# Kernel optimization log

Hardware: AMD Instinct MI355X
Metric: run time of the kernel (lower is better)

## Reference

```python
import jax, jax.numpy as jnp
import numpy as np

N_LAT, N_LON = 721, 1440
N_MESH = 40962
C_IN, N_FEAT = 64, 4
HID, OUT = 256, 256
BATCH = 2


def _precompute_interp(mesh_lat, mesh_lon):
    """Vectorized version of BilinearInterpolator.__init__ precompute."""
    lat_min, lon_min = -np.pi / 2, 0.0
    dlat = np.pi / (N_LAT - 1)
    dlon = 2 * np.pi / N_LON
    lon = np.mod(mesh_lon - lon_min, 2 * np.pi) + lon_min
    lat_idx = (mesh_lat - lat_min) / dlat
    lon_idx = (lon - lon_min) / dlon
    i0 = np.clip(np.floor(lat_idx).astype(np.int64), 0, N_LAT - 2)
    j0 = np.clip(np.floor(lon_idx).astype(np.int64), 0, N_LON - 2)
    i1 = i0 + 1
    j1 = (j0 + 1) % N_LON
    lf = np.clip(lat_idx - i0, 0.0, 1.0)
    jf = np.clip(lon_idx - j0, 0.0, 1.0)
    idx = np.stack([i0 * N_LON + j0, i0 * N_LON + j1,
                    i1 * N_LON + j0, i1 * N_LON + j1], axis=1)
    w = np.stack([(1 - lf) * (1 - jf), (1 - lf) * jf,
                  lf * (1 - jf), lf * jf], axis=1).astype(np.float32)
    return idx, w


def setup_inputs() -> dict:
    key = jax.random.key(0)
    k = jax.random.split(key, 6)
    rng = np.random.default_rng(0)
    mesh_lat = rng.uniform(-np.pi / 2 + 1e-3, np.pi / 2 - 1e-3, N_MESH)
    mesh_lon = rng.uniform(0.0, 2 * np.pi, N_MESH)
    idx, w = _precompute_interp(mesh_lat, mesh_lon)
    d_in = C_IN + N_FEAT
    return {
        "grid_data": jax.random.normal(k[0], (BATCH, N_LAT, N_LON, C_IN), jnp.float32),
        "mesh_features": jax.random.normal(k[1], (N_MESH, N_FEAT), jnp.float32),
        "indices": jnp.asarray(idx, jnp.int64 if jax.config.read('jax_enable_x64') else jnp.int32),
        "weights": jnp.asarray(w),
        "W1": jax.random.normal(k[2], (d_in, HID), jnp.float32) / np.sqrt(d_in),
        "b1": jnp.zeros((HID,), jnp.float32),
        "W2": jax.random.normal(k[3], (HID, OUT), jnp.float32) / np.sqrt(HID),
        "b2": jnp.zeros((OUT,), jnp.float32),
    }


def reference(grid_data, mesh_features, indices, weights, W1, b1, W2, b2):
    B, n_lat, n_lon, C = grid_data.shape
    grid_flat = grid_data.reshape(B, n_lat * n_lon, C)          # (B, G, C)
    corner = grid_flat[:, indices, :]                           # (B, M, 4, C)
    mesh_data = jnp.einsum('bmkc,mk->bmc', corner, weights)     # weighted 4-pt sum
    mf = jnp.broadcast_to(mesh_features[None], (B,) + mesh_features.shape)
    combined = jnp.concatenate([mesh_data, mf], axis=-1)        # (B, M, C+F)
    h = jax.nn.relu(combined @ W1 + b1)                         # 2-layer MLP
    return h @ W2 + b2                                          # (B, M, OUT)
```

## Files before the change

kernel.cpp:

```cpp
#include <hip/hip_runtime.h>
#include <hip/hip_bf16.h>


constexpr int kNLat  = 721;
constexpr int kNLon  = 1440;
constexpr long long kNPix = (long long)kNLat * kNLon;
constexpr int kMesh  = 40962;
constexpr int kCIn   = 64;
constexpr int kFeat  = 4;
constexpr int kDIn   = kCIn + kFeat;
constexpr int kHid   = 256;
constexpr int kOut   = 256;
constexpr int kBatch = 2;

constexpr int kPts    = kBatch * kMesh;
constexpr int kPtsPad = (kPts + 63) & ~63;

typedef __attribute__((ext_vector_type(8))) short bf16x8;
typedef __attribute__((ext_vector_type(4))) float f32x4;

constexpr int    WSA1_N   = 16 * 3 * 64 * 8;
constexpr int    WSB2_N   = 16 * 8 * 64 * 8;
constexpr size_t WS_BYTES = (size_t)(WSA1_N + WSB2_N) * 2;

constexpr int MP    = 64;
constexpr int NBLKB = kPtsPad / MP;
constexpr int CSTR  = 104;
constexpr int HSTR  = 264;

__device__ inline ushort f2b(float v) {
    __hip_bfloat16 h = __float2bfloat16(v);
    return *reinterpret_cast<ushort*>(&h);
}

__global__ __launch_bounds__(256)
void g2m_prep(const float* __restrict__ W1, const float* __restrict__ W2,
              ushort* __restrict__ ws) {
    const int tid = blockIdx.x * 256 + threadIdx.x;
    if (tid < 3072) {
        const int l  = tid & 63;
        const int g  = tid >> 6;
        const int ks = g % 3;
        const int rt = g / 3;
        const int hid = rt * 16 + (l & 15);
        const int k0  = ks * 32 + (l >> 4) * 8;
        ushort tmp[8];
        #pragma unroll
        for (int j = 0; j < 8; ++j) {
            const int k = k0 + j;
            tmp[j] = f2b(k < kDIn ? W1[(size_t)k * kHid + hid] : 0.f);
        }
        *reinterpret_cast<bf16x8*>(ws + (size_t)tid * 8) =
            *reinterpret_cast<bf16x8*>(tmp);
    } else if (tid < 11264) {
        const int q  = tid - 3072;
        const int l  = q & 63;
        const int g  = q >> 6;
        const int ks = g % 8;
        const int ct = g / 8;
        const int col = ct * 16 + (l & 15);
        const int k0  = ks * 32 + (l >> 4) * 8;
        ushort tmp[8];
        #pragma unroll
        for (int j = 0; j < 8; ++j) {
            const int k = k0 + j;
            tmp[j] = f2b(W2[(size_t)k * kOut + col]);
        }
        *reinterpret_cast<bf16x8*>(ws + (size_t)(WSA1_N + q * 8)) =
            *reinterpret_cast<bf16x8*>(tmp);
    }
}

__global__ __launch_bounds__(256, 3)
void g2m_fused2(const float* __restrict__ grid,
                const float* __restrict__ mfeat,
                const int*   __restrict__ indices,
                const float* __restrict__ weights,
                const float* __restrict__ b1,
                const float* __restrict__ b2,
                const ushort* __restrict__ ws,
                float* __restrict__ out)
{
    __shared__ __align__(16) ushort comb[MP * CSTR];
    __shared__ __align__(16) ushort hbuf[MP * HSTR];

    const int t    = threadIdx.x;
    const int lane = t & 63;
    const int w    = t >> 6;
    const int p0   = blockIdx.x * MP;
    const int l15  = lane & 15;
    const int l4   = lane >> 4;

    {
        const int q = l4;
        #pragma unroll
        for (int it = 0; it < 4; ++it) {
            const int row = (w * 4 + it) * 4 + q;
            const int p   = p0 + row;
            float4 acc = {0.f, 0.f, 0.f, 0.f};
            float mf0 = 0.f, mf1 = 0.f;
            if (p < kPts) {
                const int b = (p >= kMesh) ? 1 : 0;
                const int m = p - b * kMesh;
                const int4   id = *reinterpret_cast<const int4*>(indices + (size_t)m * 4);
                const float4 wt = *reinterpret_cast<const float4*>(weights + (size_t)m * 4);
                const float* gb = grid + (size_t)b * (size_t)(kNPix * kCIn);
                const float4 r0 = *reinterpret_cast<const float4*>(gb + (size_t)id.x * kCIn + l15 * 4);
                const float4 r1 = *reinterpret_cast<const float4*>(gb + (size_t)id.y * kCIn + l15 * 4);
                const float4 r2 = *reinterpret_cast<const float4*>(gb + (size_t)id.z * kCIn + l15 * 4);
                const float4 r3 = *reinterpret_cast<const float4*>(gb + (size_t)id.w * kCIn + l15 * 4);
                acc.x = fmaf(wt.x, r0.x, fmaf(wt.y, r1.x, fmaf(wt.z, r2.x, wt.w * r3.x)));
                acc.y = fmaf(wt.x, r0.y, fmaf(wt.y, r1.y, fmaf(wt.z, r2.y, wt.w * r3.y)));
                acc.z = fmaf(wt.x, r0.z, fmaf(wt.y, r1.z, fmaf(wt.z, r2.z, wt.w * r3.z)));
                acc.w = fmaf(wt.x, r0.w, fmaf(wt.y, r1.w, fmaf(wt.z, r2.w, wt.w * r3.w)));
                if (l15 < 2) {
                    mf0 = mfeat[(size_t)m * kFeat + l15 * 2];
                    mf1 = mfeat[(size_t)m * kFeat + l15 * 2 + 1];
                }
            }
            ushort* rowp = &comb[row * CSTR];
            ushort4 pk;
            pk.x = f2b(acc.x); pk.y = f2b(acc.y); pk.z = f2b(acc.z); pk.w = f2b(acc.w);
            *reinterpret_cast<ushort4*>(rowp + l15 * 4) = pk;
            ushort2 ft;
            ft.x = f2b(mf0); ft.y = f2b(mf1);
            *reinterpret_cast<ushort2*>(rowp + 64 + l15 * 2) = ft;
        }
    }
    __syncthreads();

    {
        f32x4 acc1[4][4];
        #pragma unroll
        for (int r = 0; r < 4; ++r)
            #pragma unroll
            for (int mt = 0; mt < 4; ++mt) acc1[r][mt] = (f32x4)0.f;

        #pragma unroll
        for (int ks = 0; ks < 3; ++ks) {
            bf16x8 af[4], bfr[4];
            #pragma unroll
            for (int r = 0; r < 4; ++r) {
                const int rt = w * 4 + r;
                af[r] = *reinterpret_cast<const bf16x8*>(
                            ws + (size_t)((rt * 3 + ks) * 64 + lane) * 8);
            }
            #pragma unroll
            for (int mt = 0; mt < 4; ++mt)
                bfr[mt] = *reinterpret_cast<const bf16x8*>(
                            &comb[(mt * 16 + l15) * CSTR + ks * 32 + l4 * 8]);
            #pragma unroll
            for (int r = 0; r < 4; ++r)
                #pragma unroll
                for (int mt = 0; mt < 4; ++mt)
                    acc1[r][mt] = __builtin_amdgcn_mfma_f32_16x16x32_bf16(
                                      af[r], bfr[mt], acc1[r][mt], 0, 0, 0);
        }

        #pragma unroll
        for (int r = 0; r < 4; ++r) {
            const int hid0 = (w * 4 + r) * 16 + l4 * 4;
            const float4 bv = *reinterpret_cast<const float4*>(b1 + hid0);
            #pragma unroll
            for (int mt = 0; mt < 4; ++mt) {
                const int m = mt * 16 + l15;
                ushort4 hv;
                hv.x = f2b(fmaxf(acc1[r][mt][0] + bv.x, 0.f));
                hv.y = f2b(fmaxf(acc1[r][mt][1] + bv.y, 0.f));
                hv.z = f2b(fmaxf(acc1[r][mt][2] + bv.z, 0.f));
                hv.w = f2b(fmaxf(acc1[r][mt][3] + bv.w, 0.f));
                *reinterpret_cast<ushort4*>(&hbuf[m * HSTR + hid0]) = hv;
            }
        }
    }
    __syncthreads();

    {
        f32x4 acc2[4][4];
        #pragma unroll
        for (int mt = 0; mt < 4; ++mt)
            #pragma unroll
            for (int c = 0; c < 4; ++c) acc2[mt][c] = (f32x4)0.f;

        #pragma unroll
        for (int ks = 0; ks < 8; ++ks) {
            bf16x8 hf[4], wf[4];
            #pragma unroll
            for (int mt = 0; mt < 4; ++mt)
                hf[mt] = *reinterpret_cast<const bf16x8*>(
                            &hbuf[(mt * 16 + l15) * HSTR + ks * 32 + l4 * 8]);
            #pragma unroll
            for (int c = 0; c < 4; ++c) {
                const int ct = w * 4 + c;
                wf[c] = *reinterpret_cast<const bf16x8*>(
                            ws + (size_t)(WSA1_N + ((ct * 8 + ks) * 64 + lane) * 8));
            }
            #pragma unroll
            for (int mt = 0; mt < 4; ++mt)
                #pragma unroll
                for (int c = 0; c < 4; ++c)
                    acc2[mt][c] = __builtin_amdgcn_mfma_f32_16x16x32_bf16(
                                      wf[c], hf[mt], acc2[mt][c], 0, 0, 0);
        }

        #pragma unroll
        for (int c = 0; c < 4; ++c) {
            const int col0 = (w * 4 + c) * 16 + l4 * 4;
            const float4 bv = *reinterpret_cast<const float4*>(b2 + col0);
            #pragma unroll
            for (int mt = 0; mt < 4; ++mt) {
                const int p = p0 + mt * 16 + l15;
                if (p < kPts) {
                    float4 o;
                    o.x = acc2[mt][c][0] + bv.x;
                    o.y = acc2[mt][c][1] + bv.y;
                    o.z = acc2[mt][c][2] + bv.z;
                    o.w = acc2[mt][c][3] + bv.w;
                    *reinterpret_cast<float4*>(out + (size_t)p * kOut + col0) = o;
                }
            }
        }
    }
}

extern "C" void kernel_launch(void* const* d_in, const int* in_sizes, int n_in,
                              void* d_out, int out_size, void* d_ws, size_t ws_size,
                              hipStream_t stream) {
    const float* grid    = (const float*)d_in[0];
    const float* mfeat   = (const float*)d_in[1];
    const int*   indices = (const int*)d_in[2];
    const float* weights = (const float*)d_in[3];
    const float* W1      = (const float*)d_in[4];
    const float* b1      = (const float*)d_in[5];
    const float* W2      = (const float*)d_in[6];
    const float* b2      = (const float*)d_in[7];
    float* o = (float*)d_out;

    if (ws_size >= WS_BYTES) {
        ushort* ws = (ushort*)d_ws;
        g2m_prep<<<44, 256, 0, stream>>>(W1, W2, ws);
        g2m_fused2<<<NBLKB, 256, 0, stream>>>(grid, mfeat, indices, weights,
                                              b1, b2, ws, o);
    }
}
```

Measured before the change: 51.81 us.

## Gather interpolated inputs straight into MFMA B-fragments and swizzle hidden buffer

Each wave now gathers and interpolates its own 16 mesh points directly into the register layout of the layer-1 MFMA B operand. This removes the comb shared-memory staging buffer and one barrier. Each wave then computes all 16 hidden row-tiles for its points, which means every wave reads the full W1 fragment set rather than a quarter of it. The hidden buffer drops its padding in favour of an XOR swizzle to avoid LDS bank conflicts, and the launch bound is raised to 4 blocks per CU to fit the lower LDS and register use.

```diff
diff --git a/kernel.cpp b/kernel.cpp
--- a/kernel.cpp
+++ b/kernel.cpp
@@ -25,13 +25,14 @@
 
 constexpr int MP    = 64;
 constexpr int NBLKB = kPtsPad / MP;
-constexpr int CSTR  = 104;
-constexpr int HSTR  = 264;
+constexpr int HSTR  = 256;
 
 __device__ inline ushort f2b(float v) {
     __hip_bfloat16 h = __float2bfloat16(v);
     return *reinterpret_cast<ushort*>(&h);
 }
+
+__device__ inline int hswz(int r, int c) { return r * HSTR + (c ^ ((r & 7) << 3)); }
 
 __global__ __launch_bounds__(256)
 void g2m_prep(const float* __restrict__ W1, const float* __restrict__ W2,
@@ -71,8 +72,8 @@
     }
 }
 
-__global__ __launch_bounds__(256, 3)
-void g2m_fused2(const float* __restrict__ grid,
+__global__ __launch_bounds__(256, 4)
+void g2m_fused4(const float* __restrict__ grid,
                 const float* __restrict__ mfeat,
                 const int*   __restrict__ indices,
                 const float* __restrict__ weights,
@@ -81,7 +82,6 @@
                 const ushort* __restrict__ ws,
                 float* __restrict__ out)
 {
-    __shared__ __align__(16) ushort comb[MP * CSTR];
     __shared__ __align__(16) ushort hbuf[MP * HSTR];
 
     const int t    = threadIdx.x;
@@ -91,86 +91,81 @@
     const int l15  = lane & 15;
     const int l4   = lane >> 4;
 
+    bf16x8 bA[3];
     {
-        const int q = l4;
-        #pragma unroll
-        for (int it = 0; it < 4; ++it) {
-            const int row = (w * 4 + it) * 4 + q;
-            const int p   = p0 + row;
-            float4 acc = {0.f, 0.f, 0.f, 0.f};
-            float mf0 = 0.f, mf1 = 0.f;
-            if (p < kPts) {
-                const int b = (p >= kMesh) ? 1 : 0;
-                const int m = p - b * kMesh;
-                const int4   id = *reinterpret_cast<const int4*>(indices + (size_t)m * 4);
-                const float4 wt = *reinterpret_cast<const float4*>(weights + (size_t)m * 4);
-                const float* gb = grid + (size_t)b * (size_t)(kNPix * kCIn);
-                const float4 r0 = *reinterpret_cast<const float4*>(gb + (size_t)id.x * kCIn + l15 * 4);
-                const float4 r1 = *reinterpret_cast<const float4*>(gb + (size_t)id.y * kCIn + l15 * 4);
-                const float4 r2 = *reinterpret_cast<const float4*>(gb + (size_t)id.z * kCIn + l15 * 4);
-                const float4 r3 = *reinterpret_cast<const float4*>(gb + (size_t)id.w * kCIn + l15 * 4);
-                acc.x = fmaf(wt.x, r0.x, fmaf(wt.y, r1.x, fmaf(wt.z, r2.x, wt.w * r3.x)));
-                acc.y = fmaf(wt.x, r0.y, fmaf(wt.y, r1.y, fmaf(wt.z, r2.y, wt.w * r3.y)));
-                acc.z = fmaf(wt.x, r0.z, fmaf(wt.y, r1.z, fmaf(wt.z, r2.z, wt.w * r3.z)));
-                acc.w = fmaf(wt.x, r0.w, fmaf(wt.y, r1.w, fmaf(wt.z, r2.w, wt.w * r3.w)));
-                if (l15 < 2) {
-                    mf0 = mfeat[(size_t)m * kFeat + l15 * 2];
-                    mf1 = mfeat[(size_t)m * kFeat + l15 * 2 + 1];
-                }
+        const int p = p0 + w * 16 + l15;
+        float4 r0a{0,0,0,0}, r0b{0,0,0,0}, r0c{0,0,0,0}, r0d{0,0,0,0};
+        float4 r1a{0,0,0,0}, r1b{0,0,0,0}, r1c{0,0,0,0}, r1d{0,0,0,0};
+        float4 r2a{0,0,0,0}, r2b{0,0,0,0}, r2c{0,0,0,0}, r2d{0,0,0,0};
+        float4 r3a{0,0,0,0}, r3b{0,0,0,0}, r3c{0,0,0,0}, r3d{0,0,0,0};
+        float4 wt{0,0,0,0}, mfv{0,0,0,0};
+        if (p < kPts) {
+            const int b = (p >= kMesh) ? 1 : 0;
+            const int m = p - b * kMesh;
+            const int4 id = *reinterpret_cast<const int4*>(indices + (size_t)m * 4);
+            wt = *reinterpret_cast<const float4*>(weights + (size_t)m * 4);
+            const float* gb = grid + (size_t)b * (size_t)(kNPix * kCIn);
+            const int o0 = l4 * 8;
+            const int o1 = 32 + l4 * 8;
+            const float* c0 = gb + (size_t)id.x * kCIn;
+            const float* c1 = gb + (size_t)id.y * kCIn;
+            const float* c2 = gb + (size_t)id.z * kCIn;
+            const float* c3 = gb + (size_t)id.w * kCIn;
+            r0a = *reinterpret_cast<const float4*>(c0 + o0);
+            r0b = *reinterpret_cast<const float4*>(c0 + o0 + 4);
+            r0c = *reinterpret_cast<const float4*>(c0 + o1);
+            r0d = *reinterpret_cast<const float4*>(c0 + o1 + 4);
+            r1a = *reinterpret_cast<const float4*>(c1 + o0);
+            r1b = *reinterpret_cast<const float4*>(c1 + o0 + 4);
+            r1c = *reinterpret_cast<const float4*>(c1 + o1);
+            r1d = *reinterpret_cast<const float4*>(c1 + o1 + 4);
+            r2a = *reinterpret_cast<const float4*>(c2 + o0);
+            r2b = *reinterpret_cast<const float4*>(c2 + o0 + 4);
+            r2c = *reinterpret_cast<const float4*>(c2 + o1);
+            r2d = *reinterpret_cast<const float4*>(c2 + o1 + 4);
+            r3a = *reinterpret_cast<const float4*>(c3 + o0);
+            r3b = *reinterpret_cast<const float4*>(c3 + o0 + 4);
+            r3c = *reinterpret_cast<const float4*>(c3 + o1);
+            r3d = *reinterpret_cast<const float4*>(c3 + o1 + 4);
+            if (l4 == 0) mfv = *reinterpret_cast<const float4*>(mfeat + (size_t)m * 4);
+        }
+        ushort f0[8], f1[8], f2[8];
+        #pragma unroll
+        for (int j = 0; j < 4; ++j) {
+            const float a0 = (&r0a.x)[j], a1 = (&r1a.x)[j], a2 = (&r2a.x)[j], a3 = (&r3a.x)[j];
+            f0[j] = f2b(fmaf(wt.x, a0, fmaf(wt.y, a1, fmaf(wt.z, a2, wt.w * a3))));
+            const float b0 = (&r0b.x)[j], b1v = (&r1b.x)[j], b2v = (&r2b.x)[j], b3 = (&r3b.x)[j];
+            f0[4 + j] = f2b(fmaf(wt.x, b0, fmaf(wt.y, b1v, fmaf(wt.z, b2v, wt.w * b3))));
+            const float c0v = (&r0c.x)[j], c1v = (&r1c.x)[j], c2v = (&r2c.x)[j], c3v = (&r3c.x)[j];
+            f1[j] = f2b(fmaf(wt.x, c0v, fmaf(wt.y, c1v, fmaf(wt.z, c2v, wt.w * c3v))));
+            const float d0 = (&r0d.x)[j], d1 = (&r1d.x)[j], d2 = (&r2d.x)[j], d3 = (&r3d.x)[j];
+            f1[4 + j] = f2b(fmaf(wt.x, d0, fmaf(wt.y, d1, fmaf(wt.z, d2, wt.w * d3))));
+            f2[j]     = f2b((&mfv.x)[j]);
+            f2[4 + j] = 0;
+        }
+        bA[0] = *reinterpret_cast<bf16x8*>(f0);
+        bA[1] = *reinterpret_cast<bf16x8*>(f1);
+        bA[2] = *reinterpret_cast<bf16x8*>(f2);
+    }
+
+    {
+        #pragma unroll
+        for (int rt = 0; rt < 16; ++rt) {
+            f32x4 acc = (f32x4)0.f;
+            #pragma unroll
+            for (int ks = 0; ks < 3; ++ks) {
+                const bf16x8 af = *reinterpret_cast<const bf16x8*>(
+                        ws + (size_t)((rt * 3 + ks) * 64 + lane) * 8);
+                acc = __builtin_amdgcn_mfma_f32_16x16x32_bf16(af, bA[ks], acc, 0, 0, 0);
             }
-            ushort* rowp = &comb[row * CSTR];
-            ushort4 pk;
-            pk.x = f2b(acc.x); pk.y = f2b(acc.y); pk.z = f2b(acc.z); pk.w = f2b(acc.w);
-            *reinterpret_cast<ushort4*>(rowp + l15 * 4) = pk;
-            ushort2 ft;
-            ft.x = f2b(mf0); ft.y = f2b(mf1);
-            *reinterpret_cast<ushort2*>(rowp + 64 + l15 * 2) = ft;
-        }
-    }
-    __syncthreads();
-
-    {
-        f32x4 acc1[4][4];
-        #pragma unroll
-        for (int r = 0; r < 4; ++r)
-            #pragma unroll
-            for (int mt = 0; mt < 4; ++mt) acc1[r][mt] = (f32x4)0.f;
-
-        #pragma unroll
-        for (int ks = 0; ks < 3; ++ks) {
-            bf16x8 af[4], bfr[4];
-            #pragma unroll
-            for (int r = 0; r < 4; ++r) {
-                const int rt = w * 4 + r;
-                af[r] = *reinterpret_cast<const bf16x8*>(
-                            ws + (size_t)((rt * 3 + ks) * 64 + lane) * 8);
-            }
-            #pragma unroll
-            for (int mt = 0; mt < 4; ++mt)
-                bfr[mt] = *reinterpret_cast<const bf16x8*>(
-                            &comb[(mt * 16 + l15) * CSTR + ks * 32 + l4 * 8]);
-            #pragma unroll
-            for (int r = 0; r < 4; ++r)
-                #pragma unroll
-                for (int mt = 0; mt < 4; ++mt)
-                    acc1[r][mt] = __builtin_amdgcn_mfma_f32_16x16x32_bf16(
-                                      af[r], bfr[mt], acc1[r][mt], 0, 0, 0);
-        }
-
-        #pragma unroll
-        for (int r = 0; r < 4; ++r) {
-            const int hid0 = (w * 4 + r) * 16 + l4 * 4;
+            const int hid0 = rt * 16 + l4 * 4;
             const float4 bv = *reinterpret_cast<const float4*>(b1 + hid0);
-            #pragma unroll
-            for (int mt = 0; mt < 4; ++mt) {
-                const int m = mt * 16 + l15;
-                ushort4 hv;
-                hv.x = f2b(fmaxf(acc1[r][mt][0] + bv.x, 0.f));
-                hv.y = f2b(fmaxf(acc1[r][mt][1] + bv.y, 0.f));
-                hv.z = f2b(fmaxf(acc1[r][mt][2] + bv.z, 0.f));
-                hv.w = f2b(fmaxf(acc1[r][mt][3] + bv.w, 0.f));
-                *reinterpret_cast<ushort4*>(&hbuf[m * HSTR + hid0]) = hv;
-            }
+            ushort4 hv;
+            hv.x = f2b(fmaxf(acc[0] + bv.x, 0.f));
+            hv.y = f2b(fmaxf(acc[1] + bv.y, 0.f));
+            hv.z = f2b(fmaxf(acc[2] + bv.z, 0.f));
+            hv.w = f2b(fmaxf(acc[3] + bv.w, 0.f));
+            *reinterpret_cast<ushort4*>(&hbuf[hswz(w * 16 + l15, hid0)]) = hv;
         }
     }
     __syncthreads();
@@ -188,7 +183,7 @@
             #pragma unroll
             for (int mt = 0; mt < 4; ++mt)
                 hf[mt] = *reinterpret_cast<const bf16x8*>(
-                            &hbuf[(mt * 16 + l15) * HSTR + ks * 32 + l4 * 8]);
+                            &hbuf[hswz(mt * 16 + l15, ks * 32 + l4 * 8)]);
             #pragma unroll
             for (int c = 0; c < 4; ++c) {
                 const int ct = w * 4 + c;
@@ -239,7 +234,7 @@
     if (ws_size >= WS_BYTES) {
         ushort* ws = (ushort*)d_ws;
         g2m_prep<<<44, 256, 0, stream>>>(W1, W2, ws);
-        g2m_fused2<<<NBLKB, 256, 0, stream>>>(grid, mfeat, indices, weights,
+        g2m_fused4<<<NBLKB, 256, 0, stream>>>(grid, mfeat, indices, weights,
                                               b1, b2, ws, o);
     }
 }
```

Result: slower. 55.91 us (+7.9%).

## Warp-specialize into gather producers and MFMA consumers with double-buffered tiles

Applied to the files above, without the earlier changes.

Replaces the one-tile-per-block fused kernel with a persistent 512-thread kernel over 512 blocks. Four producer waves gather and interpolate the next 64-point tile into a second shared buffer while four consumer waves run both MLP GEMMs on the current tile. Each block handles 2 or 3 tiles. The aim is to hide the random-gather latency behind MFMA work. In exchange, half the waves issue the gathers, tile counts per block are uneven, and each tile step needs two block-wide barriers. The padding columns of the staging buffer are also zeroed explicitly.

```diff
diff --git a/kernel.cpp b/kernel.cpp
--- a/kernel.cpp
+++ b/kernel.cpp
@@ -23,10 +23,11 @@
 constexpr int    WSB2_N   = 16 * 8 * 64 * 8;
 constexpr size_t WS_BYTES = (size_t)(WSA1_N + WSB2_N) * 2;
 
-constexpr int MP    = 64;
-constexpr int NBLKB = kPtsPad / MP;
-constexpr int CSTR  = 104;
-constexpr int HSTR  = 264;
+constexpr int MP     = 64;
+constexpr int NTILES = kPtsPad / MP;
+constexpr int NBLK   = 512;
+constexpr int CSTR   = 104;
+constexpr int HSTR   = 264;
 
 __device__ inline ushort f2b(float v) {
     __hip_bfloat16 h = __float2bfloat16(v);
@@ -71,155 +72,220 @@
     }
 }
 
-__global__ __launch_bounds__(256, 3)
-void g2m_fused2(const float* __restrict__ grid,
-                const float* __restrict__ mfeat,
-                const int*   __restrict__ indices,
-                const float* __restrict__ weights,
-                const float* __restrict__ b1,
-                const float* __restrict__ b2,
-                const ushort* __restrict__ ws,
-                float* __restrict__ out)
+struct PState {
+    float4 rr[4][4];
+    float4 wt[4];
+    float  mf0[4], mf1[4];
+};
+
+__device__ inline void prod_load(const float* __restrict__ grid,
+                                 const float* __restrict__ mfeat,
+                                 const int*   __restrict__ indices,
+                                 const float* __restrict__ weights,
+                                 int p0, int pw, int l15, int l4, PState& s) {
+    #pragma unroll
+    for (int it = 0; it < 4; ++it) {
+        const int p = p0 + pw * 16 + it * 4 + l4;
+        s.rr[it][0] = s.rr[it][1] = s.rr[it][2] = s.rr[it][3] = float4{0.f, 0.f, 0.f, 0.f};
+        s.wt[it] = float4{0.f, 0.f, 0.f, 0.f};
+        s.mf0[it] = 0.f; s.mf1[it] = 0.f;
+        if (p < kPts) {
+            const int b = (p >= kMesh) ? 1 : 0;
+            const int m = p - b * kMesh;
+            const int4 id = *reinterpret_cast<const int4*>(indices + (size_t)m * 4);
+            s.wt[it] = *reinterpret_cast<const float4*>(weights + (size_t)m * 4);
+            const float* gb = grid + (size_t)b * (size_t)(kNPix * kCIn);
+            s.rr[it][0] = *reinterpret_cast<const float4*>(gb + (size_t)id.x * kCIn + l15 * 4);
+            s.rr[it][1] = *reinterpret_cast<const float4*>(gb + (size_t)id.y * kCIn + l15 * 4);
+            s.rr[it][2] = *reinterpret_cast<const float4*>(gb + (size_t)id.z * kCIn + l15 * 4);
+            s.rr[it][3] = *reinterpret_cast<const float4*>(gb + (size_t)id.w * kCIn + l15 * 4);
+            if (l15 < 2) {
+                s.mf0[it] = mfeat[(size_t)m * kFeat + l15 * 2];
+                s.mf1[it] = mfeat[(size_t)m * kFeat + l15 * 2 + 1];
+            }
+        }
+    }
+}
+
+__device__ inline void prod_reduce(const PState& s, ushort* comb,
+                                   int pw, int l15, int l4) {
+    #pragma unroll
+    for (int it = 0; it < 4; ++it) {
+        const int row = pw * 16 + it * 4 + l4;
+        const float4 wt = s.wt[it];
+        float4 acc;
+        acc.x = fmaf(wt.x, s.rr[it][0].x, fmaf(wt.y, s.rr[it][1].x, fmaf(wt.z, s.rr[it][2].x, wt.w * s.rr[it][3].x)));
+        acc.y = fmaf(wt.x, s.rr[it][0].y, fmaf(wt.y, s.rr[it][1].y, fmaf(wt.z, s.rr[it][2].y, wt.w * s.rr[it][3].y)));
+        acc.z = fmaf(wt.x, s.rr[it][0].z, fmaf(wt.y, s.rr[it][1].z, fmaf(wt.z, s.rr[it][2].z, wt.w * s.rr[it][3].z)));
+        acc.w = fmaf(wt.x, s.rr[it][0].w, fmaf(wt.y, s.rr[it][1].w, fmaf(wt.z, s.rr[it][2].w, wt.w * s.rr[it][3].w)));
+        ushort4 pk;
+        pk.x = f2b(acc.x); pk.y = f2b(acc.y); pk.z = f2b(acc.z); pk.w = f2b(acc.w);
+        *reinterpret_cast<ushort4*>(&comb[row * CSTR + l15 * 4]) = pk;
+        ushort2 ft;
+        ft.x = f2b(s.mf0[it]); ft.y = f2b(s.mf1[it]);
+        *reinterpret_cast<ushort2*>(&comb[row * CSTR + 64 + l15 * 2]) = ft;
+        if (l15 < (CSTR - kDIn) / 2 && l15 >= 0) {  }
+    }
+    #pragma unroll
+    for (int it = 0; it < 4; ++it) {
+        const int row = pw * 16 + it * 4 + l4;
+        if (l15 < 14) comb[row * CSTR + 68 + l15 * 2] = 0;
+        if (l15 < 14) comb[row * CSTR + 69 + l15 * 2] = 0;
+    }
+}
+
+__device__ inline void gemm1(const ushort* comb, ushort* hbuf,
+                             const ushort* __restrict__ ws,
+                             const float* __restrict__ b1,
+                             int cw, int lane, int l15, int l4) {
+    f32x4 acc1[4][4];
+    #pragma unroll
+    for (int r = 0; r < 4; ++r)
+        #pragma unroll
+        for (int mt = 0; mt < 4; ++mt) acc1[r][mt] = (f32x4)0.f;
+
+    #pragma unroll
+    for (int ks = 0; ks < 3; ++ks) {
+        bf16x8 af[4], bfr[4];
+        #pragma unroll
+        for (int r = 0; r < 4; ++r) {
+            const int rt = cw * 4 + r;
+            af[r] = *reinterpret_cast<const bf16x8*>(
+                        ws + (size_t)((rt * 3 + ks) * 64 + lane) * 8);
+        }
+        #pragma unroll
+        for (int mt = 0; mt < 4; ++mt)
+            bfr[mt] = *reinterpret_cast<const bf16x8*>(
+                        &comb[(mt * 16 + l15) * CSTR + ks * 32 + l4 * 8]);
+        #pragma unroll
+        for (int r = 0; r < 4; ++r)
+            #pragma unroll
+            for (int mt = 0; mt < 4; ++mt)
+                acc1[r][mt] = __builtin_amdgcn_mfma_f32_16x16x32_bf16(
+                                  af[r], bfr[mt], acc1[r][mt], 0, 0, 0);
+    }
+
+    #pragma unroll
+    for (int r = 0; r < 4; ++r) {
+        const int hid0 = (cw * 4 + r) * 16 + l4 * 4;
+        const float4 bv = *reinterpret_cast<const float4*>(b1 + hid0);
+        #pragma unroll
+        for (int mt = 0; mt < 4; ++mt) {
+            const int m = mt * 16 + l15;
+            ushort4 hv;
+            hv.x = f2b(fmaxf(acc1[r][mt][0] + bv.x, 0.f));
+            hv.y = f2b(fmaxf(acc1[r][mt][1] + bv.y, 0.f));
+            hv.z = f2b(fmaxf(acc1[r][mt][2] + bv.z, 0.f));
+            hv.w = f2b(fmaxf(acc1[r][mt][3] + bv.w, 0.f));
+            *reinterpret_cast<ushort4*>(&hbuf[m * HSTR + hid0]) = hv;
+        }
+    }
+}
+
+__device__ inline void gemm2(const ushort* hbuf,
+                             const ushort* __restrict__ ws,
+                             const float* __restrict__ b2,
+                             float* __restrict__ out,
+                             int p0, int cw, int lane, int l15, int l4) {
+    f32x4 acc2[4][4];
+    #pragma unroll
+    for (int mt = 0; mt < 4; ++mt)
+        #pragma unroll
+        for (int c = 0; c < 4; ++c) acc2[mt][c] = (f32x4)0.f;
+
+    #pragma unroll
+    for (int ks = 0; ks < 8; ++ks) {
+        bf16x8 hf[4], wf[4];
+        #pragma unroll
+        for (int mt = 0; mt < 4; ++mt)
+            hf[mt] = *reinterpret_cast<const bf16x8*>(
+                        &hbuf[(mt * 16 + l15) * HSTR + ks * 32 + l4 * 8]);
+        #pragma unroll
+        for (int c = 0; c < 4; ++c) {
+            const int ct = cw * 4 + c;
+            wf[c] = *reinterpret_cast<const bf16x8*>(
+                        ws + (size_t)(WSA1_N + ((ct * 8 + ks) * 64 + lane) * 8));
+        }
+        #pragma unroll
+        for (int mt = 0; mt < 4; ++mt)
+            #pragma unroll
+            for (int c = 0; c < 4; ++c)
+                acc2[mt][c] = __builtin_amdgcn_mfma_f32_16x16x32_bf16(
+                                  wf[c], hf[mt], acc2[mt][c], 0, 0, 0);
+    }
+
+    #pragma unroll
+    for (int c = 0; c < 4; ++c) {
+        const int col0 = (cw * 4 + c) * 16 + l4 * 4;
+        const float4 bv = *reinterpret_cast<const float4*>(b2 + col0);
+        #pragma unroll
+        for (int mt = 0; mt < 4; ++mt) {
+            const int p = p0 + mt * 16 + l15;
+            if (p < kPts) {
+                float4 o;
+                o.x = acc2[mt][c][0] + bv.x;
+                o.y = acc2[mt][c][1] + bv.y;
+                o.z = acc2[mt][c][2] + bv.z;
+                o.w = acc2[mt][c][3] + bv.w;
+                *reinterpret_cast<float4*>(out + (size_t)p * kOut + col0) = o;
+            }
+        }
+    }
+}
+
+__global__ __launch_bounds__(512, 2)
+void g2m_pc(const float* __restrict__ grid,
+            const float* __restrict__ mfeat,
+            const int*   __restrict__ indices,
+            const float* __restrict__ weights,
+            const float* __restrict__ b1,
+            const float* __restrict__ b2,
+            const ushort* __restrict__ ws,
+            float* __restrict__ out)
 {
-    __shared__ __align__(16) ushort comb[MP * CSTR];
+    __shared__ __align__(16) ushort combA[MP * CSTR];
+    __shared__ __align__(16) ushort combB[MP * CSTR];
     __shared__ __align__(16) ushort hbuf[MP * HSTR];
 
     const int t    = threadIdx.x;
     const int lane = t & 63;
-    const int w    = t >> 6;
-    const int p0   = blockIdx.x * MP;
+    const int wv   = t >> 6;
+    const bool isP = wv < 4;
+    const int rw   = wv & 3;
     const int l15  = lane & 15;
     const int l4   = lane >> 4;
-
-    {
-        const int q = l4;
-        #pragma unroll
-        for (int it = 0; it < 4; ++it) {
-            const int row = (w * 4 + it) * 4 + q;
-            const int p   = p0 + row;
-            float4 acc = {0.f, 0.f, 0.f, 0.f};
-            float mf0 = 0.f, mf1 = 0.f;
-            if (p < kPts) {
-                const int b = (p >= kMesh) ? 1 : 0;
-                const int m = p - b * kMesh;
-                const int4   id = *reinterpret_cast<const int4*>(indices + (size_t)m * 4);
-                const float4 wt = *reinterpret_cast<const float4*>(weights + (size_t)m * 4);
-                const float* gb = grid + (size_t)b * (size_t)(kNPix * kCIn);
-                const float4 r0 = *reinterpret_cast<const float4*>(gb + (size_t)id.x * kCIn + l15 * 4);
-                const float4 r1 = *reinterpret_cast<const float4*>(gb + (size_t)id.y * kCIn + l15 * 4);
-                const float4 r2 = *reinterpret_cast<const float4*>(gb + (size_t)id.z * kCIn + l15 * 4);
-                const float4 r3 = *reinterpret_cast<const float4*>(gb + (size_t)id.w * kCIn + l15 * 4);
-                acc.x = fmaf(wt.x, r0.x, fmaf(wt.y, r1.x, fmaf(wt.z, r2.x, wt.w * r3.x)));
-                acc.y = fmaf(wt.x, r0.y, fmaf(wt.y, r1.y, fmaf(wt.z, r2.y, wt.w * r3.y)));
-                acc.z = fmaf(wt.x, r0.z, fmaf(wt.y, r1.z, fmaf(wt.z, r2.z, wt.w * r3.z)));
-                acc.w = fmaf(wt.x, r0.w, fmaf(wt.y, r1.w, fmaf(wt.z, r2.w, wt.w * r3.w)));
-                if (l15 < 2) {
-                    mf0 = mfeat[(size_t)m * kFeat + l15 * 2];
-                    mf1 = mfeat[(size_t)m * kFeat + l15 * 2 + 1];
-                }
-            }
-            ushort* rowp = &comb[row * CSTR];
-            ushort4 pk;
-            pk.x = f2b(acc.x); pk.y = f2b(acc.y); pk.z = f2b(acc.z); pk.w = f2b(acc.w);
-            *reinterpret_cast<ushort4*>(rowp + l15 * 4) = pk;
-            ushort2 ft;
-            ft.x = f2b(mf0); ft.y = f2b(mf1);
-            *reinterpret_cast<ushort2*>(rowp + 64 + l15 * 2) = ft;
-        }
+    const int bid  = blockIdx.x;
+    const int nt   = (bid < NTILES - 2 * NBLK) ? 3 : 2;
+
+    PState s;
+
+    if (isP) {
+        prod_load(grid, mfeat, indices, weights, bid * MP, rw, l15, l4, s);
+        prod_reduce(s, combA, rw, l15, l4);
     }
     __syncthreads();
 
-    {
-        f32x4 acc1[4][4];
-        #pragma unroll
-        for (int r = 0; r < 4; ++r)
-            #pragma unroll
-            for (int mt = 0; mt < 4; ++mt) acc1[r][mt] = (f32x4)0.f;
-
-        #pragma unroll
-        for (int ks = 0; ks < 3; ++ks) {
-            bf16x8 af[4], bfr[4];
-            #pragma unroll
-            for (int r = 0; r < 4; ++r) {
-                const int rt = w * 4 + r;
-                af[r] = *reinterpret_cast<const bf16x8*>(
-                            ws + (size_t)((rt * 3 + ks) * 64 + lane) * 8);
-            }
-            #pragma unroll
-            for (int mt = 0; mt < 4; ++mt)
-                bfr[mt] = *reinterpret_cast<const bf16x8*>(
-                            &comb[(mt * 16 + l15) * CSTR + ks * 32 + l4 * 8]);
-            #pragma unroll
-            for (int r = 0; r < 4; ++r)
-                #pragma unroll
-                for (int mt = 0; mt < 4; ++mt)
-                    acc1[r][mt] = __builtin_amdgcn_mfma_f32_16x16x32_bf16(
-                                      af[r], bfr[mt], acc1[r][mt], 0, 0, 0);
-        }
-
-        #pragma unroll
-        for (int r = 0; r < 4; ++r) {
-            const int hid0 = (w * 4 + r) * 16 + l4 * 4;
-            const float4 bv = *reinterpret_cast<const float4*>(b1 + hid0);
-            #pragma unroll
-            for (int mt = 0; mt < 4; ++mt) {
-                const int m = mt * 16 + l15;
-                ushort4 hv;
-                hv.x = f2b(fmaxf(acc1[r][mt][0] + bv.x, 0.f));
-                hv.y = f2b(fmaxf(acc1[r][mt][1] + bv.y, 0.f));
-                hv.z = f2b(fmaxf(acc1[r][mt][2] + bv.z, 0.f));
-                hv.w = f2b(fmaxf(acc1[r][mt][3] + bv.w, 0.f));
-                *reinterpret_cast<ushort4*>(&hbuf[m * HSTR + hid0]) = hv;
-            }
-        }
-    }
-    __syncthreads();
-
-    {
-        f32x4 acc2[4][4];
-        #pragma unroll
-        for (int mt = 0; mt < 4; ++mt)
-            #pragma unroll
-            for (int c = 0; c < 4; ++c) acc2[mt][c] = (f32x4)0.f;
-
-        #pragma unroll
-        for (int ks = 0; ks < 8; ++ks) {
-            bf16x8 hf[4], wf[4];
-            #pragma unroll
-            for (int mt = 0; mt < 4; ++mt)
-                hf[mt] = *reinterpret_cast<const bf16x8*>(
-                            &hbuf[(mt * 16 + l15) * HSTR + ks * 32 + l4 * 8]);
-            #pragma unroll
-            for (int c = 0; c < 4; ++c) {
-                const int ct = w * 4 + c;
-                wf[c] = *reinterpret_cast<const bf16x8*>(
-                            ws + (size_t)(WSA1_N + ((ct * 8 + ks) * 64 + lane) * 8));
-            }
-            #pragma unroll
-            for (int mt = 0; mt < 4; ++mt)
-                #pragma unroll
-                for (int c = 0; c < 4; ++c)
-                    acc2[mt][c] = __builtin_amdgcn_mfma_f32_16x16x32_bf16(
-                                      wf[c], hf[mt], acc2[mt][c], 0, 0, 0);
-        }
-
-        #pragma unroll
-        for (int c = 0; c < 4; ++c) {
-            const int col0 = (w * 4 + c) * 16 + l4 * 4;
-            const float4 bv = *reinterpret_cast<const float4*>(b2 + col0);
-            #pragma unroll
-            for (int mt = 0; mt < 4; ++mt) {
-                const int p = p0 + mt * 16 + l15;
-                if (p < kPts) {
-                    float4 o;
-                    o.x = acc2[mt][c][0] + bv.x;
-                    o.y = acc2[mt][c][1] + bv.y;
-                    o.z = acc2[mt][c][2] + bv.z;
-                    o.w = acc2[mt][c][3] + bv.w;
-                    *reinterpret_cast<float4*>(out + (size_t)p * kOut + col0) = o;
-                }
-            }
-        }
+    for (int j = 0; j < nt; ++j) {
+        ushort* cur = (j & 1) ? combB : combA;
+        ushort* nxt = (j & 1) ? combA : combB;
+        const int p0 = (bid + j * NBLK) * MP;
+
+        if (isP) {
+            if (j + 1 < nt)
+                prod_load(grid, mfeat, indices, weights,
+                          (bid + (j + 1) * NBLK) * MP, rw, l15, l4, s);
+        } else {
+            gemm1(cur, hbuf, ws, b1, rw, lane, l15, l4);
+        }
+        __syncthreads();
+
+        if (isP) {
+            if (j + 1 < nt)
+                prod_reduce(s, nxt, rw, l15, l4);
+        } else {
+            gemm2(hbuf, ws, b2, out, p0, rw, lane, l15, l4);
+        }
+        __syncthreads();
     }
 }
 
@@ -239,7 +305,7 @@
     if (ws_size >= WS_BYTES) {
         ushort* ws = (ushort*)d_ws;
         g2m_prep<<<44, 256, 0, stream>>>(W1, W2, ws);
-        g2m_fused2<<<NBLKB, 256, 0, stream>>>(grid, mfeat, indices, weights,
-                                              b1, b2, ws, o);
-    }
-}
+        g2m_pc<<<NBLK, 512, 0, stream>>>(grid, mfeat, indices, weights,
+                                         b1, b2, ws, o);
+    }
+}
```

Result: slower. 108.3 us (+109.1%).

## Make each wave own 16 points end-to-end with swizzled private LDS

Applied to the files above, without the earlier changes.

Restructures the fused gather+MLP kernel so that each wave handles its own 16 mesh points through both matmul layers. The new layout drops the block-wide __syncthreads and uses a per-wave XOR-swizzled LDS tile instead of padded shared arrays. It raises the occupancy hint to 4 and writes the output with nontemporal stores. In exchange each wave now streams the full W1/W2 weight fragments from global/L2 (four times more weight traffic per block), with less MFMA operand reuse per load.

```diff
diff --git a/kernel.cpp b/kernel.cpp
--- a/kernel.cpp
+++ b/kernel.cpp
@@ -23,15 +23,15 @@
 constexpr int    WSB2_N   = 16 * 8 * 64 * 8;
 constexpr size_t WS_BYTES = (size_t)(WSA1_N + WSB2_N) * 2;
 
-constexpr int MP    = 64;
-constexpr int NBLKB = kPtsPad / MP;
-constexpr int CSTR  = 104;
-constexpr int HSTR  = 264;
+constexpr int NBLKB = kPtsPad / 64;
+constexpr int HSTR  = 256;
 
 __device__ inline ushort f2b(float v) {
     __hip_bfloat16 h = __float2bfloat16(v);
     return *reinterpret_cast<ushort*>(&h);
 }
+
+__device__ inline int swz(int r, int c) { return r * HSTR + (c ^ ((r & 7) << 3)); }
 
 __global__ __launch_bounds__(256)
 void g2m_prep(const float* __restrict__ W1, const float* __restrict__ W2,
@@ -71,31 +71,31 @@
     }
 }
 
-__global__ __launch_bounds__(256, 3)
-void g2m_fused2(const float* __restrict__ grid,
-                const float* __restrict__ mfeat,
-                const int*   __restrict__ indices,
-                const float* __restrict__ weights,
-                const float* __restrict__ b1,
-                const float* __restrict__ b2,
-                const ushort* __restrict__ ws,
-                float* __restrict__ out)
+__global__ __launch_bounds__(256, 4)
+void g2m_wave(const float* __restrict__ grid,
+              const float* __restrict__ mfeat,
+              const int*   __restrict__ indices,
+              const float* __restrict__ weights,
+              const float* __restrict__ b1,
+              const float* __restrict__ b2,
+              const ushort* __restrict__ ws,
+              float* __restrict__ out)
 {
-    __shared__ __align__(16) ushort comb[MP * CSTR];
-    __shared__ __align__(16) ushort hbuf[MP * HSTR];
+    __shared__ __align__(16) ushort lds[4][16 * HSTR];
 
     const int t    = threadIdx.x;
     const int lane = t & 63;
     const int w    = t >> 6;
-    const int p0   = blockIdx.x * MP;
     const int l15  = lane & 15;
     const int l4   = lane >> 4;
+    const int p0   = blockIdx.x * 64 + w * 16;
+    ushort* my = lds[w];
 
     {
         const int q = l4;
         #pragma unroll
         for (int it = 0; it < 4; ++it) {
-            const int row = (w * 4 + it) * 4 + q;
+            const int row = it * 4 + q;
             const int p   = p0 + row;
             float4 acc = {0.f, 0.f, 0.f, 0.f};
             float mf0 = 0.f, mf1 = 0.f;
@@ -118,107 +118,65 @@
                     mf1 = mfeat[(size_t)m * kFeat + l15 * 2 + 1];
                 }
             }
-            ushort* rowp = &comb[row * CSTR];
             ushort4 pk;
             pk.x = f2b(acc.x); pk.y = f2b(acc.y); pk.z = f2b(acc.z); pk.w = f2b(acc.w);
-            *reinterpret_cast<ushort4*>(rowp + l15 * 4) = pk;
+            *reinterpret_cast<ushort4*>(&my[swz(row, l15 * 4)]) = pk;
             ushort2 ft;
             ft.x = f2b(mf0); ft.y = f2b(mf1);
-            *reinterpret_cast<ushort2*>(rowp + 64 + l15 * 2) = ft;
-        }
-    }
-    __syncthreads();
-
-    {
-        f32x4 acc1[4][4];
-        #pragma unroll
-        for (int r = 0; r < 4; ++r)
-            #pragma unroll
-            for (int mt = 0; mt < 4; ++mt) acc1[r][mt] = (f32x4)0.f;
-
+            *reinterpret_cast<ushort2*>(&my[swz(row, 64 + l15 * 2)]) = ft;
+        }
+    }
+
+    bf16x8 bfr[3];
+    #pragma unroll
+    for (int ks = 0; ks < 3; ++ks)
+        bfr[ks] = *reinterpret_cast<const bf16x8*>(&my[swz(l15, ks * 32 + l4 * 8)]);
+
+    #pragma unroll 4
+    for (int rt = 0; rt < 16; ++rt) {
+        f32x4 acc = (f32x4)0.f;
         #pragma unroll
         for (int ks = 0; ks < 3; ++ks) {
-            bf16x8 af[4], bfr[4];
-            #pragma unroll
-            for (int r = 0; r < 4; ++r) {
-                const int rt = w * 4 + r;
-                af[r] = *reinterpret_cast<const bf16x8*>(
-                            ws + (size_t)((rt * 3 + ks) * 64 + lane) * 8);
-            }
-            #pragma unroll
-            for (int mt = 0; mt < 4; ++mt)
-                bfr[mt] = *reinterpret_cast<const bf16x8*>(
-                            &comb[(mt * 16 + l15) * CSTR + ks * 32 + l4 * 8]);
-            #pragma unroll
-            for (int r = 0; r < 4; ++r)
-                #pragma unroll
-                for (int mt = 0; mt < 4; ++mt)
-                    acc1[r][mt] = __builtin_amdgcn_mfma_f32_16x16x32_bf16(
-                                      af[r], bfr[mt], acc1[r][mt], 0, 0, 0);
-        }
-
-        #pragma unroll
-        for (int r = 0; r < 4; ++r) {
-            const int hid0 = (w * 4 + r) * 16 + l4 * 4;
-            const float4 bv = *reinterpret_cast<const float4*>(b1 + hid0);
-            #pragma unroll
-            for (int mt = 0; mt < 4; ++mt) {
-                const int m = mt * 16 + l15;
-                ushort4 hv;
-                hv.x = f2b(fmaxf(acc1[r][mt][0] + bv.x, 0.f));
-                hv.y = f2b(fmaxf(acc1[r][mt][1] + bv.y, 0.f));
-                hv.z = f2b(fmaxf(acc1[r][mt][2] + bv.z, 0.f));
-                hv.w = f2b(fmaxf(acc1[r][mt][3] + bv.w, 0.f));
-                *reinterpret_cast<ushort4*>(&hbuf[m * HSTR + hid0]) = hv;
-            }
-        }
-    }
-    __syncthreads();
-
-    {
-        f32x4 acc2[4][4];
-        #pragma unroll
-        for (int mt = 0; mt < 4; ++mt)
-            #pragma unroll
-            for (int c = 0; c < 4; ++c) acc2[mt][c] = (f32x4)0.f;
-
+            const bf16x8 af = *reinterpret_cast<const bf16x8*>(
+                    ws + (size_t)((rt * 3 + ks) * 64 + lane) * 8);
+            acc = __builtin_amdgcn_mfma_f32_16x16x32_bf16(af, bfr[ks], acc, 0, 0, 0);
+        }
+        const int hid0 = rt * 16 + l4 * 4;
+        const float4 bv = *reinterpret_cast<const float4*>(b1 + hid0);
+        ushort4 hv;
+        hv.x = f2b(fmaxf(acc[0] + bv.x, 0.f));
+        hv.y = f2b(fmaxf(acc[1] + bv.y, 0.f));
+        hv.z = f2b(fmaxf(acc[2] + bv.z, 0.f));
+        hv.w = f2b(fmaxf(acc[3] + bv.w, 0.f));
+        *reinterpret_cast<ushort4*>(&my[swz(l15, hid0)]) = hv;
+    }
+
+    bf16x8 hf[8];
+    #pragma unroll
+    for (int ks = 0; ks < 8; ++ks)
+        hf[ks] = *reinterpret_cast<const bf16x8*>(&my[swz(l15, ks * 32 + l4 * 8)]);
+
+    const int p   = p0 + l15;
+    const bool ok = (p < kPts);
+    float* obase  = out + (size_t)p * kOut;
+    #pragma unroll 2
+    for (int ct = 0; ct < 16; ++ct) {
+        f32x4 acc = (f32x4)0.f;
         #pragma unroll
         for (int ks = 0; ks < 8; ++ks) {
-            bf16x8 hf[4], wf[4];
-            #pragma unroll
-            for (int mt = 0; mt < 4; ++mt)
-                hf[mt] = *reinterpret_cast<const bf16x8*>(
-                            &hbuf[(mt * 16 + l15) * HSTR + ks * 32 + l4 * 8]);
-            #pragma unroll
-            for (int c = 0; c < 4; ++c) {
-                const int ct = w * 4 + c;
-                wf[c] = *reinterpret_cast<const bf16x8*>(
-                            ws + (size_t)(WSA1_N + ((ct * 8 + ks) * 64 + lane) * 8));
-            }
-            #pragma unroll
-            for (int mt = 0; mt < 4; ++mt)
-                #pragma unroll
-                for (int c = 0; c < 4; ++c)
-                    acc2[mt][c] = __builtin_amdgcn_mfma_f32_16x16x32_bf16(
-                                      wf[c], hf[mt], acc2[mt][c], 0, 0, 0);
-        }
-
-        #pragma unroll
-        for (int c = 0; c < 4; ++c) {
-            const int col0 = (w * 4 + c) * 16 + l4 * 4;
-            const float4 bv = *reinterpret_cast<const float4*>(b2 + col0);
-            #pragma unroll
-            for (int mt = 0; mt < 4; ++mt) {
-                const int p = p0 + mt * 16 + l15;
-                if (p < kPts) {
-                    float4 o;
-                    o.x = acc2[mt][c][0] + bv.x;
-                    o.y = acc2[mt][c][1] + bv.y;
-                    o.z = acc2[mt][c][2] + bv.z;
-                    o.w = acc2[mt][c][3] + bv.w;
-                    *reinterpret_cast<float4*>(out + (size_t)p * kOut + col0) = o;
-                }
-            }
+            const bf16x8 wf = *reinterpret_cast<const bf16x8*>(
+                    ws + (size_t)(WSA1_N + ((ct * 8 + ks) * 64 + lane) * 8));
+            acc = __builtin_amdgcn_mfma_f32_16x16x32_bf16(wf, hf[ks], acc, 0, 0, 0);
+        }
+        const int col0 = ct * 16 + l4 * 4;
+        const float4 bv = *reinterpret_cast<const float4*>(b2 + col0);
+        if (ok) {
+            f32x4 o;
+            o[0] = acc[0] + bv.x;
+            o[1] = acc[1] + bv.y;
+            o[2] = acc[2] + bv.z;
+            o[3] = acc[3] + bv.w;
+            __builtin_nontemporal_store(o, reinterpret_cast<f32x4*>(obase + col0));
         }
     }
 }
@@ -239,7 +197,7 @@
     if (ws_size >= WS_BYTES) {
         ushort* ws = (ushort*)d_ws;
         g2m_prep<<<44, 256, 0, stream>>>(W1, W2, ws);
-        g2m_fused2<<<NBLKB, 256, 0, stream>>>(grid, mfeat, indices, weights,
-                                              b1, b2, ws, o);
-    }
-}
+        g2m_wave<<<NBLKB, 256, 0, stream>>>(grid, mfeat, indices, weights,
+                                            b1, b2, ws, o);
+    }
+}
```

Measured after the change: 66.99 us. 29.3% more time.
